# Optimization experiments

Measured on AMD Instinct MI355X. Metric: run time of the kernel, lower is better.

## Reference

```python
import jax, jax.numpy as jnp
import numpy as np

B, L, D, H = 2, 2048, 2048, 16
DH = D // H

def setup_inputs() -> dict:
    key = jax.random.key(0)
    ks = jax.random.split(key, 12)
    def w(k):
        return jax.random.normal(k, (D, D), dtype=jnp.float32) * 0.02
    def b(k):
        return jax.random.normal(k, (D,), dtype=jnp.float32) * 0.02
    return {
        'q': jax.random.normal(ks[0], (B, L, D), dtype=jnp.float32),
        'k': jax.random.normal(ks[1], (B, L, D), dtype=jnp.float32),
        'v': jax.random.normal(ks[2], (B, L, D), dtype=jnp.float32),
        'Wq': w(ks[3]), 'bq': b(ks[4]),
        'Wk': w(ks[5]), 'bk': b(ks[6]),
        'Wv': w(ks[7]), 'bv': b(ks[8]),
        'Wo': w(ks[9]), 'bo': b(ks[10]),
    }

def reference(q, k, v, Wq, bq, Wk, bk, Wv, bv, Wo, bo):
    # Linear projections (torch Linear: x @ W.T + b)
    qh = q @ Wq.T + bq
    kh = k @ Wk.T + bk
    vh = v @ Wv.T + bv
    # b l (h d) -> b h l d
    def split(x):
        b_, l_, _ = x.shape
        return x.reshape(b_, l_, H, DH).transpose(0, 2, 1, 3)
    qh, kh, vh = split(qh), split(kh), split(vh)
    # Faithful to source: scores = q @ k^T / d_head**(-0.5) == q @ k^T * sqrt(d_head)
    scale = jnp.float32(DH) ** 0.5
    scores = jnp.einsum('bhid,bhjd->bhij', qh, kh) * scale
    causal = jnp.triu(jnp.ones((L, L), dtype=jnp.float32), 1)  # triu(1) mask
    scores = scores - causal * 1e7
    attn = jax.nn.softmax(scores, axis=-1)
    out = jnp.einsum('bhij,bhjd->bhid', attn, vh)
    out = out.transpose(0, 2, 1, 3).reshape(B, L, D)  # b h l d -> b l (h d)
    return out @ Wo.T + bo
```

## Files before the change

### kernel.cpp

```cpp
#include <hip/hip_runtime.h>

typedef unsigned short u16;
typedef _Float16 hfrag __attribute__((ext_vector_type(8)));
typedef float f32x4 __attribute__((ext_vector_type(4)));

#define MFMA16F __builtin_amdgcn_mfma_f32_16x16x32_f16

__device__ __forceinline__ u16 f2h(float f) {
  return __builtin_bit_cast(u16, (_Float16)f);
}
__device__ __forceinline__ void splith(float x, u16 &h, u16 &l) {
  _Float16 hh = (_Float16)x;
  _Float16 ll = (_Float16)(x - (float)hh);
  h = __builtin_bit_cast(u16, hh);
  l = __builtin_bit_cast(u16, ll);
}

__device__ __forceinline__ void gl2lds16(const void* g, void* l) {
  __builtin_amdgcn_global_load_lds(
      (const __attribute__((address_space(1))) unsigned int*)g,
      (__attribute__((address_space(3))) unsigned int*)l, 16, 0, 0);
}

__global__ void precvt_h(const float* __restrict__ W, u16* __restrict__ hi)
{
  size_t i = ((size_t)blockIdx.x * 256 + threadIdx.x) * 4;
  float4 x = *(const float4*)(W + i);
  ushort4 h;
  h.x = f2h(x.x); h.y = f2h(x.y); h.z = f2h(x.z); h.w = f2h(x.w);
  *(ushort4*)(hi + i) = h;
}

template<int EMIT>
__global__ __launch_bounds__(256, 2)
void gemm_qk(const float* __restrict__ A, const u16* __restrict__ Wh_g,
             const float* __restrict__ bias,
             u16* __restrict__ ohi, u16* __restrict__ olo)
{
  __shared__ u16 Ahi[128][40];
  __shared__ u16 Alo[128][40];
  __shared__ u16 Whs[128 * 32];

  const int tid = threadIdx.x, wave = tid >> 6, lane = tid & 63;
  const int quad = lane >> 4, l16 = lane & 15;
  const int bm = blockIdx.y * 128, bn = blockIdx.x * 128;
  const int wm = (wave >> 1) * 64, wn = (wave & 1) * 64;
  const int rl = lane >> 2, cb = lane & 3;

  f32x4 acc[4][4] = {};

  for (int k0 = 0; k0 < 2048; k0 += 32) {
    __syncthreads();
#pragma unroll
    for (int i = 0; i < 2; ++i) {
      int r0 = wave * 32 + i * 16;
      gl2lds16(Wh_g + (size_t)(bn + r0 + rl) * 2048 + k0 + cb * 8,
               &Whs[r0 * 32]);
    }
#pragma unroll
    for (int it = 0; it < 4; ++it) {
      int idx = tid + it * 256;
      int row = idx >> 3, c4 = (idx & 7) << 2;
      float4 av = *(const float4*)(A + (size_t)(bm + row) * 2048 + k0 + c4);
      ushort4 h, l;
      splith(av.x, h.x, l.x); splith(av.y, h.y, l.y);
      splith(av.z, h.z, l.z); splith(av.w, h.w, l.w);
      *(ushort4*)&Ahi[row][c4] = h;
      *(ushort4*)&Alo[row][c4] = l;
    }
    __syncthreads();

    hfrag ah[4], al_[4], wh[4];
#pragma unroll
    for (int i = 0; i < 4; ++i) {
      ah[i]  = *(const hfrag*)&Ahi[wm + i * 16 + l16][quad * 8];
      al_[i] = *(const hfrag*)&Alo[wm + i * 16 + l16][quad * 8];
      wh[i]  = *(const hfrag*)&Whs[(wn + i * 16 + l16) * 32 + quad * 8];
    }
#pragma unroll
    for (int mi = 0; mi < 4; ++mi)
#pragma unroll
      for (int ni = 0; ni < 4; ++ni) {
        acc[mi][ni] = MFMA16F(ah[mi],  wh[ni], acc[mi][ni], 0, 0, 0);
        acc[mi][ni] = MFMA16F(al_[mi], wh[ni], acc[mi][ni], 0, 0, 0);
      }
  }

  const float SCALE = 11.31370849898476f;
#pragma unroll
  for (int ni = 0; ni < 4; ++ni) {
    int n_g = bn + wn + ni * 16 + l16;
    float bv = bias[n_g];
#pragma unroll
    for (int mi = 0; mi < 4; ++mi)
#pragma unroll
      for (int r = 0; r < 4; ++r) {
        int m_g = bm + wm + mi * 16 + quad * 4 + r;
        float v = acc[mi][ni][r] + bv;
        int b = m_g >> 11, ll = m_g & 2047, hh = n_g >> 7, dh = n_g & 127;
        size_t off = (((size_t)(b * 16 + hh)) * 2048 + ll) * 128 + dh;
        if constexpr (EMIT == 0) {
          v *= SCALE;
          u16 h, l; splith(v, h, l);
          ohi[off] = h; olo[off] = l;
        } else {
          ohi[off] = f2h(v);
        }
      }
  }
}

template<int AMODE, int OUTM>
__global__ __launch_bounds__(256, 2)
void gemm_pl(const void* __restrict__ Ap, const float* __restrict__ W,
             const float* __restrict__ bias, void* __restrict__ outp)
{
  __shared__ u16 As[128 * 40];
  __shared__ u16 Ws[128][40];

  const int tid = threadIdx.x, wave = tid >> 6, lane = tid & 63;
  const int quad = lane >> 4, l16 = lane & 15;
  const int bm = blockIdx.y * 128, bn = blockIdx.x * 128;
  const int wm = (wave >> 1) * 64, wn = (wave & 1) * 64;
  const int rl = lane >> 2, cb = lane & 3;
  constexpr int ASTRIDE = (AMODE == 1) ? 32 : 40;

  f32x4 acc[4][4] = {};

  for (int k0 = 0; k0 < 2048; k0 += 32) {
    __syncthreads();
    if constexpr (AMODE == 1) {
      const u16* Ah = (const u16*)Ap;
#pragma unroll
      for (int i = 0; i < 2; ++i) {
        int r0 = wave * 32 + i * 16;
        gl2lds16(Ah + (size_t)(bm + r0 + rl) * 2048 + k0 + cb * 8,
                 &As[r0 * 32]);
      }
    }
#pragma unroll
    for (int it = 0; it < 4; ++it) {
      int idx = tid + it * 256;
      int row = idx >> 3, c4 = (idx & 7) << 2;
      float4 wv = *(const float4*)(W + (size_t)(bn + row) * 2048 + k0 + c4);
      ushort4 h;
      h.x = f2h(wv.x); h.y = f2h(wv.y); h.z = f2h(wv.z); h.w = f2h(wv.w);
      *(ushort4*)&Ws[row][c4] = h;
      if constexpr (AMODE == 0) {
        const float* A = (const float*)Ap;
        float4 av = *(const float4*)(A + (size_t)(bm + row) * 2048 + k0 + c4);
        ushort4 ha;
        ha.x = f2h(av.x); ha.y = f2h(av.y); ha.z = f2h(av.z); ha.w = f2h(av.w);
        *(ushort4*)&As[row * 40 + c4] = ha;
      }
    }
    __syncthreads();

    hfrag af[4], wf[4];
#pragma unroll
    for (int i = 0; i < 4; ++i) {
      af[i] = *(const hfrag*)&As[(wm + i * 16 + l16) * ASTRIDE + quad * 8];
      wf[i] = *(const hfrag*)&Ws[wn + i * 16 + l16][quad * 8];
    }
    if constexpr (OUTM == 1) {
#pragma unroll
      for (int mi = 0; mi < 4; ++mi)
#pragma unroll
        for (int ni = 0; ni < 4; ++ni)
          acc[mi][ni] = MFMA16F(wf[mi], af[ni], acc[mi][ni], 0, 0, 0);
    } else {
#pragma unroll
      for (int mi = 0; mi < 4; ++mi)
#pragma unroll
        for (int ni = 0; ni < 4; ++ni)
          acc[mi][ni] = MFMA16F(af[mi], wf[ni], acc[mi][ni], 0, 0, 0);
    }
  }

  if constexpr (OUTM == 1) {
#pragma unroll
    for (int mi = 0; mi < 4; ++mi)
#pragma unroll
      for (int r = 0; r < 4; ++r) {
        int dim = bn + wn + mi * 16 + quad * 4 + r;
        float bv = bias[dim];
        int hh = dim >> 7, dh = dim & 127;
#pragma unroll
        for (int ni = 0; ni < 4; ++ni) {
          int tok = bm + wm + ni * 16 + l16;
          int b = tok >> 11, l = tok & 2047;
          ((u16*)outp)[(((size_t)(b * 16 + hh)) * 128 + dh) * 2048 + l] =
              f2h(acc[mi][ni][r] + bv);
        }
      }
  } else {
#pragma unroll
    for (int ni = 0; ni < 4; ++ni) {
      int n_g = bn + wn + ni * 16 + l16;
      float bv = bias[n_g];
#pragma unroll
      for (int mi = 0; mi < 4; ++mi)
#pragma unroll
        for (int r = 0; r < 4; ++r) {
          int m_g = bm + wm + mi * 16 + quad * 4 + r;
          ((float*)outp)[(size_t)m_g * 2048 + n_g] = acc[mi][ni][r] + bv;
        }
    }
  }
}

__global__ __launch_bounds__(256, 1)
void attn_k(const u16* __restrict__ qhi_g, const u16* __restrict__ qlo_g,
            const u16* __restrict__ khi_g, const u16* __restrict__ vT,
            u16* __restrict__ Ow)
{
  __shared__ u16 KhiB[2][64 * 128];
  __shared__ u16 VTB[2][128 * 64];
  __shared__ u16 PmA[4][32][72];

  const int tid = threadIdx.x, wave = tid >> 6, lane = tid & 63;
  const int quad = lane >> 4, l16 = lane & 15;
  const int bh = blockIdx.x & 31, qx = blockIdx.x >> 5;
  const u16* Qhb = qhi_g + (size_t)bh * 2048 * 128;
  const u16* Qlb = qlo_g + (size_t)bh * 2048 * 128;
  const u16* Khb = khi_g + (size_t)bh * 2048 * 128;
  const u16* Vb  = vT    + (size_t)bh * 128 * 2048;

  const int krl = lane >> 4, kpb = lane & 15;
  const int vrl = lane >> 3, vpb = lane & 7;

  hfrag ones;
#pragma unroll
  for (int j = 0; j < 8; ++j) ones[j] = (_Float16)1.0f;

  auto stage = [&](int kv0, int bsel) {
#pragma unroll
    for (int i = 0; i < 4; ++i) {
      int r = wave * 16 + i * 4 + krl;
      int j = kpb ^ (r & 15);
      gl2lds16(Khb + (size_t)(kv0 + r) * 128 + j * 8,
               &KhiB[bsel][(wave * 16 + i * 4) * 128]);
      int rv = wave * 32 + i * 8 + vrl;
      int jv = vpb ^ (rv & 7);
      gl2lds16(Vb + (size_t)rv * 2048 + kv0 + jv * 8,
               &VTB[bsel][(wave * 32 + i * 8) * 64]);
    }
  };

  const int b = bh >> 4, h = bh & 15;

#pragma unroll 1
  for (int ph = 0; ph < 2; ++ph) {
    const int qt = (ph == 0) ? qx : 15 - qx;
    const int qrow0 = qt * 128 + wave * 32;
    const int nkv = 2 * (qt + 1);

    stage(0, 0);

    hfrag qhf[2][4], qlf[2][4];
#pragma unroll
    for (int t = 0; t < 2; ++t)
#pragma unroll
      for (int f = 0; f < 4; ++f) {
        size_t off = (size_t)(qrow0 + t * 16 + l16) * 128 + f * 32 + quad * 8;
        qhf[t][f] = *(const hfrag*)(Qhb + off);
        qlf[t][f] = *(const hfrag*)(Qlb + off);
      }

    float mprev[2] = {-3e38f, -3e38f};
    f32x4 o[2][9] = {};

#pragma unroll 1
    for (int kt = 0; kt < nkv; ++kt) {
      const int kv0 = kt * 64, bsel = kt & 1;
      __syncthreads();
      if (kt + 1 < nkv) stage((kt + 1) * 64, 1 - bsel);

      if (kv0 <= qrow0 + 31) {
        f32x4 st[4][2] = {};
#pragma unroll
        for (int f = 0; f < 4; ++f)
#pragma unroll
          for (int c = 0; c < 4; ++c) {
            int poff = (c * 16 + l16) * 128 + (((f * 4 + quad) ^ l16) << 3);
            hfrag kf = *(const hfrag*)&KhiB[bsel][poff];
#pragma unroll
            for (int t = 0; t < 2; ++t) {
              st[c][t] = MFMA16F(kf, qhf[t][f], st[c][t], 0, 0, 0);
              st[c][t] = MFMA16F(kf, qlf[t][f], st[c][t], 0, 0, 0);
            }
          }

        const bool needmask = (kv0 + 64 > qrow0);
        float al2[2];
#pragma unroll
        for (int t = 0; t < 2; ++t) {
          const int rg = qrow0 + t * 16 + l16;
          if (needmask) {
#pragma unroll
            for (int c = 0; c < 4; ++c)
#pragma unroll
              for (int r = 0; r < 4; ++r)
                if (kv0 + c * 16 + quad * 4 + r > rg) st[c][t][r] = -1e7f;
          }
          float mx = st[0][t][0];
#pragma unroll
          for (int c = 0; c < 4; ++c)
#pragma unroll
            for (int r = 0; r < 4; ++r) mx = fmaxf(mx, st[c][t][r]);
          mx = fmaxf(mx, __shfl_xor(mx, 16));
          mx = fmaxf(mx, __shfl_xor(mx, 32));
          float mnew = fmaxf(mprev[t], mx);
          al2[t] = __expf(mprev[t] - mnew);
          mprev[t] = mnew;
#pragma unroll
          for (int c = 0; c < 4; ++c) {
            ushort4 pk;
            pk.x = f2h(__expf(st[c][t][0] - mnew));
            pk.y = f2h(__expf(st[c][t][1] - mnew));
            pk.z = f2h(__expf(st[c][t][2] - mnew));
            pk.w = f2h(__expf(st[c][t][3] - mnew));
            *(ushort4*)&PmA[wave][t * 16 + l16][c * 16 + quad * 4] = pk;
          }
        }
        if (__ballot(al2[0] != 1.f || al2[1] != 1.f)) {
#pragma unroll
          for (int t = 0; t < 2; ++t) {
            f32x4 av;
            av[0] = __shfl(al2[t], quad * 4 + 0);
            av[1] = __shfl(al2[t], quad * 4 + 1);
            av[2] = __shfl(al2[t], quad * 4 + 2);
            av[3] = __shfl(al2[t], quad * 4 + 3);
#pragma unroll
            for (int d = 0; d < 9; ++d) o[t][d] *= av;
          }
        }

#pragma unroll
        for (int k2 = 0; k2 < 2; ++k2) {
          hfrag pf0 = *(const hfrag*)&PmA[wave][l16][k2 * 32 + quad * 8];
          hfrag pf1 = *(const hfrag*)&PmA[wave][16 + l16][k2 * 32 + quad * 8];
#pragma unroll
          for (int d = 0; d < 9; ++d) {
            hfrag vf = (d < 8)
                ? *(const hfrag*)&VTB[bsel][(d * 16 + l16) * 64 +
                                            (((k2 * 4 + quad) ^ (l16 & 7)) << 3)]
                : ones;
            o[0][d] = MFMA16F(pf0, vf, o[0][d], 0, 0, 0);
            o[1][d] = MFMA16F(pf1, vf, o[1][d], 0, 0, 0);
          }
        }
      }
    }

#pragma unroll
    for (int t = 0; t < 2; ++t)
#pragma unroll
      for (int r = 0; r < 4; ++r) {
        int rg = qrow0 + t * 16 + quad * 4 + r;
        float inv = 1.f / o[t][8][r];
#pragma unroll
        for (int d = 0; d < 8; ++d)
          Ow[((size_t)(b * 2048 + rg)) * 2048 + h * 128 + d * 16 + l16] =
              f2h(o[t][d][r] * inv);
      }
  }
}

extern "C" void kernel_launch(void* const* d_in, const int* in_sizes, int n_in,
                              void* d_out, int out_size, void* d_ws, size_t ws_size,
                              hipStream_t stream) {
  const float* q  = (const float*)d_in[0];
  const float* k  = (const float*)d_in[1];
  const float* v  = (const float*)d_in[2];
  const float* Wq = (const float*)d_in[3];
  const float* bq = (const float*)d_in[4];
  const float* Wk = (const float*)d_in[5];
  const float* bk = (const float*)d_in[6];
  const float* Wv = (const float*)d_in[7];
  const float* bv = (const float*)d_in[8];
  const float* Wo = (const float*)d_in[9];
  const float* bo = (const float*)d_in[10];

  u16* ws  = (u16*)d_ws;
  u16* qHi = ws;
  u16* qLo = ws + 8388608u;
  u16* kHi = ws + 16777216u;
  u16* WH  = ws + 25165824u;
  u16* vTb = ws + 29360128u;
  u16* Owb = ws + 37748736u;

  dim3 blk(256);
  dim3 gg(16, 32);
  precvt_h<<<4096, blk, 0, stream>>>(Wq, WH);
  gemm_qk<0><<<gg, blk, 0, stream>>>(q, WH, bq, qHi, qLo);
  precvt_h<<<4096, blk, 0, stream>>>(Wk, WH);
  gemm_qk<1><<<gg, blk, 0, stream>>>(k, WH, bk, kHi, nullptr);
  gemm_pl<0, 1><<<gg, blk, 0, stream>>>(v, Wv, bv, vTb);
  attn_k<<<dim3(256), blk, 0, stream>>>(qHi, qLo, kHi, vTb, Owb);
  gemm_pl<1, 2><<<gg, blk, 0, stream>>>(Owb, Wo, bo, d_out);
}
```

Measured before the change: 638.6 us.

## Pre-convert activations to fp16 and stream all GEMM tiles via async LDS loads

Moves the fp32-to-fp16 (hi/lo split) conversion of q, k, v and all weights into separate pre-conversion kernels. Every GEMM then loads both operands with direct global-to-LDS async copies into XOR-swizzled 64-wide K tiles, halving the number of K iterations and barriers. This removes in-loop conversion ALU work and register staging, in exchange for extra full passes over the activations and extra workspace traffic, with buffers reused across stages.

Result: faster. 530.7 us (-16.9%).

```diff
diff --git a/kernel.cpp b/kernel.cpp
--- a/kernel.cpp
+++ b/kernel.cpp
@@ -31,59 +31,68 @@
   *(ushort4*)(hi + i) = h;
 }
 
+__global__ void precvt_split(const float* __restrict__ X,
+                             u16* __restrict__ hi, u16* __restrict__ lo)
+{
+  size_t i = ((size_t)blockIdx.x * 256 + threadIdx.x) * 4;
+  float4 x = *(const float4*)(X + i);
+  ushort4 h, l;
+  splith(x.x, h.x, l.x); splith(x.y, h.y, l.y);
+  splith(x.z, h.z, l.z); splith(x.w, h.w, l.w);
+  *(ushort4*)(hi + i) = h;
+  *(ushort4*)(lo + i) = l;
+}
+
 template<int EMIT>
 __global__ __launch_bounds__(256, 2)
-void gemm_qk(const float* __restrict__ A, const u16* __restrict__ Wh_g,
-             const float* __restrict__ bias,
+void gemm_qk(const u16* __restrict__ Ahi_g, const u16* __restrict__ Alo_g,
+             const u16* __restrict__ Wh_g, const float* __restrict__ bias,
              u16* __restrict__ ohi, u16* __restrict__ olo)
 {
-  __shared__ u16 Ahi[128][40];
-  __shared__ u16 Alo[128][40];
-  __shared__ u16 Whs[128 * 32];
+  __shared__ u16 AhS[128 * 64];
+  __shared__ u16 AlS[128 * 64];
+  __shared__ u16 WS[128 * 64];
 
   const int tid = threadIdx.x, wave = tid >> 6, lane = tid & 63;
   const int quad = lane >> 4, l16 = lane & 15;
   const int bm = blockIdx.y * 128, bn = blockIdx.x * 128;
   const int wm = (wave >> 1) * 64, wn = (wave & 1) * 64;
-  const int rl = lane >> 2, cb = lane & 3;
+  const int srow = lane >> 3;
+  const int jcol = ((lane & 7) ^ srow) << 3;
 
   f32x4 acc[4][4] = {};
 
-  for (int k0 = 0; k0 < 2048; k0 += 32) {
+  for (int k0 = 0; k0 < 2048; k0 += 64) {
     __syncthreads();
 #pragma unroll
-    for (int i = 0; i < 2; ++i) {
-      int r0 = wave * 32 + i * 16;
-      gl2lds16(Wh_g + (size_t)(bn + r0 + rl) * 2048 + k0 + cb * 8,
-               &Whs[r0 * 32]);
-    }
-#pragma unroll
-    for (int it = 0; it < 4; ++it) {
-      int idx = tid + it * 256;
-      int row = idx >> 3, c4 = (idx & 7) << 2;
-      float4 av = *(const float4*)(A + (size_t)(bm + row) * 2048 + k0 + c4);
-      ushort4 h, l;
-      splith(av.x, h.x, l.x); splith(av.y, h.y, l.y);
-      splith(av.z, h.z, l.z); splith(av.w, h.w, l.w);
-      *(ushort4*)&Ahi[row][c4] = h;
-      *(ushort4*)&Alo[row][c4] = l;
+    for (int i = 0; i < 4; ++i) {
+      int r0 = wave * 32 + i * 8;
+      size_t ga = (size_t)(bm + r0 + srow) * 2048 + k0 + jcol;
+      size_t gw = (size_t)(bn + r0 + srow) * 2048 + k0 + jcol;
+      gl2lds16(Ahi_g + ga, &AhS[r0 * 64]);
+      gl2lds16(Alo_g + ga, &AlS[r0 * 64]);
+      gl2lds16(Wh_g + gw, &WS[r0 * 64]);
     }
     __syncthreads();
 
-    hfrag ah[4], al_[4], wh[4];
-#pragma unroll
-    for (int i = 0; i < 4; ++i) {
-      ah[i]  = *(const hfrag*)&Ahi[wm + i * 16 + l16][quad * 8];
-      al_[i] = *(const hfrag*)&Alo[wm + i * 16 + l16][quad * 8];
-      wh[i]  = *(const hfrag*)&Whs[(wn + i * 16 + l16) * 32 + quad * 8];
-    }
-#pragma unroll
-    for (int mi = 0; mi < 4; ++mi)
-#pragma unroll
-      for (int ni = 0; ni < 4; ++ni) {
-        acc[mi][ni] = MFMA16F(ah[mi],  wh[ni], acc[mi][ni], 0, 0, 0);
-        acc[mi][ni] = MFMA16F(al_[mi], wh[ni], acc[mi][ni], 0, 0, 0);
-      }
+#pragma unroll
+    for (int kk = 0; kk < 2; ++kk) {
+      const int jr = (((kk * 4 + quad) ^ (l16 & 7)) << 3);
+      hfrag ah[4], al_[4], wh[4];
+#pragma unroll
+      for (int i = 0; i < 4; ++i) {
+        ah[i]  = *(const hfrag*)&AhS[(wm + i * 16 + l16) * 64 + jr];
+        al_[i] = *(const hfrag*)&AlS[(wm + i * 16 + l16) * 64 + jr];
+        wh[i]  = *(const hfrag*)&WS[(wn + i * 16 + l16) * 64 + jr];
+      }
+#pragma unroll
+      for (int mi = 0; mi < 4; ++mi)
+#pragma unroll
+        for (int ni = 0; ni < 4; ++ni) {
+          acc[mi][ni] = MFMA16F(ah[mi],  wh[ni], acc[mi][ni], 0, 0, 0);
+          acc[mi][ni] = MFMA16F(al_[mi], wh[ni], acc[mi][ni], 0, 0, 0);
+        }
+    }
   }
 
   const float SCALE = 11.31370849898476f;
@@ -110,70 +119,55 @@
   }
 }
 
-template<int AMODE, int OUTM>
+template<int OUTM>
 __global__ __launch_bounds__(256, 2)
-void gemm_pl(const void* __restrict__ Ap, const float* __restrict__ W,
+void gemm_pl(const u16* __restrict__ A_g, const u16* __restrict__ Wh_g,
              const float* __restrict__ bias, void* __restrict__ outp)
 {
-  __shared__ u16 As[128 * 40];
-  __shared__ u16 Ws[128][40];
+  __shared__ u16 AS[128 * 64];
+  __shared__ u16 WS[128 * 64];
 
   const int tid = threadIdx.x, wave = tid >> 6, lane = tid & 63;
   const int quad = lane >> 4, l16 = lane & 15;
   const int bm = blockIdx.y * 128, bn = blockIdx.x * 128;
   const int wm = (wave >> 1) * 64, wn = (wave & 1) * 64;
-  const int rl = lane >> 2, cb = lane & 3;
-  constexpr int ASTRIDE = (AMODE == 1) ? 32 : 40;
+  const int srow = lane >> 3;
+  const int jcol = ((lane & 7) ^ srow) << 3;
 
   f32x4 acc[4][4] = {};
 
-  for (int k0 = 0; k0 < 2048; k0 += 32) {
+  for (int k0 = 0; k0 < 2048; k0 += 64) {
     __syncthreads();
-    if constexpr (AMODE == 1) {
-      const u16* Ah = (const u16*)Ap;
-#pragma unroll
-      for (int i = 0; i < 2; ++i) {
-        int r0 = wave * 32 + i * 16;
-        gl2lds16(Ah + (size_t)(bm + r0 + rl) * 2048 + k0 + cb * 8,
-                 &As[r0 * 32]);
-      }
-    }
-#pragma unroll
-    for (int it = 0; it < 4; ++it) {
-      int idx = tid + it * 256;
-      int row = idx >> 3, c4 = (idx & 7) << 2;
-      float4 wv = *(const float4*)(W + (size_t)(bn + row) * 2048 + k0 + c4);
-      ushort4 h;
-      h.x = f2h(wv.x); h.y = f2h(wv.y); h.z = f2h(wv.z); h.w = f2h(wv.w);
-      *(ushort4*)&Ws[row][c4] = h;
-      if constexpr (AMODE == 0) {
-        const float* A = (const float*)Ap;
-        float4 av = *(const float4*)(A + (size_t)(bm + row) * 2048 + k0 + c4);
-        ushort4 ha;
-        ha.x = f2h(av.x); ha.y = f2h(av.y); ha.z = f2h(av.z); ha.w = f2h(av.w);
-        *(ushort4*)&As[row * 40 + c4] = ha;
-      }
+#pragma unroll
+    for (int i = 0; i < 4; ++i) {
+      int r0 = wave * 32 + i * 8;
+      gl2lds16(A_g  + (size_t)(bm + r0 + srow) * 2048 + k0 + jcol, &AS[r0 * 64]);
+      gl2lds16(Wh_g + (size_t)(bn + r0 + srow) * 2048 + k0 + jcol, &WS[r0 * 64]);
     }
     __syncthreads();
 
-    hfrag af[4], wf[4];
-#pragma unroll
-    for (int i = 0; i < 4; ++i) {
-      af[i] = *(const hfrag*)&As[(wm + i * 16 + l16) * ASTRIDE + quad * 8];
-      wf[i] = *(const hfrag*)&Ws[wn + i * 16 + l16][quad * 8];
-    }
-    if constexpr (OUTM == 1) {
-#pragma unroll
-      for (int mi = 0; mi < 4; ++mi)
-#pragma unroll
-        for (int ni = 0; ni < 4; ++ni)
-          acc[mi][ni] = MFMA16F(wf[mi], af[ni], acc[mi][ni], 0, 0, 0);
-    } else {
-#pragma unroll
-      for (int mi = 0; mi < 4; ++mi)
-#pragma unroll
-        for (int ni = 0; ni < 4; ++ni)
-          acc[mi][ni] = MFMA16F(af[mi], wf[ni], acc[mi][ni], 0, 0, 0);
+#pragma unroll
+    for (int kk = 0; kk < 2; ++kk) {
+      const int jr = (((kk * 4 + quad) ^ (l16 & 7)) << 3);
+      hfrag af[4], wf[4];
+#pragma unroll
+      for (int i = 0; i < 4; ++i) {
+        af[i] = *(const hfrag*)&AS[(wm + i * 16 + l16) * 64 + jr];
+        wf[i] = *(const hfrag*)&WS[(wn + i * 16 + l16) * 64 + jr];
+      }
+      if constexpr (OUTM == 1) {
+#pragma unroll
+        for (int mi = 0; mi < 4; ++mi)
+#pragma unroll
+          for (int ni = 0; ni < 4; ++ni)
+            acc[mi][ni] = MFMA16F(wf[mi], af[ni], acc[mi][ni], 0, 0, 0);
+      } else {
+#pragma unroll
+        for (int mi = 0; mi < 4; ++mi)
+#pragma unroll
+          for (int ni = 0; ni < 4; ++ni)
+            acc[mi][ni] = MFMA16F(af[mi], wf[ni], acc[mi][ni], 0, 0, 0);
+      }
     }
   }
 
@@ -382,21 +376,27 @@
   const float* Wo = (const float*)d_in[9];
   const float* bo = (const float*)d_in[10];
 
-  u16* ws  = (u16*)d_ws;
-  u16* qHi = ws;
-  u16* qLo = ws + 8388608u;
-  u16* kHi = ws + 16777216u;
-  u16* WH  = ws + 25165824u;
-  u16* vTb = ws + 29360128u;
-  u16* Owb = ws + 37748736u;
+  u16* ws   = (u16*)d_ws;
+  u16* qHi  = ws;
+  u16* qLo  = ws + 8388608u;
+  u16* kHi  = ws + 16777216u;
+  u16* WH   = ws + 25165824u;
+  u16* bufA = ws + 29360128u;
+  u16* bufB = ws + 37748736u;
 
   dim3 blk(256);
   dim3 gg(16, 32);
+
+  precvt_split<<<8192, blk, 0, stream>>>(q, bufA, bufB);
   precvt_h<<<4096, blk, 0, stream>>>(Wq, WH);
-  gemm_qk<0><<<gg, blk, 0, stream>>>(q, WH, bq, qHi, qLo);
+  gemm_qk<0><<<gg, blk, 0, stream>>>(bufA, bufB, WH, bq, qHi, qLo);
+  precvt_split<<<8192, blk, 0, stream>>>(k, bufA, bufB);
   precvt_h<<<4096, blk, 0, stream>>>(Wk, WH);
-  gemm_qk<1><<<gg, blk, 0, stream>>>(k, WH, bk, kHi, nullptr);
-  gemm_pl<0, 1><<<gg, blk, 0, stream>>>(v, Wv, bv, vTb);
-  attn_k<<<dim3(256), blk, 0, stream>>>(qHi, qLo, kHi, vTb, Owb);
-  gemm_pl<1, 2><<<gg, blk, 0, stream>>>(Owb, Wo, bo, d_out);
-}
+  gemm_qk<1><<<gg, blk, 0, stream>>>(bufA, bufB, WH, bk, kHi, nullptr);
+  precvt_h<<<8192, blk, 0, stream>>>(v, bufA);
+  precvt_h<<<4096, blk, 0, stream>>>(Wv, WH);
+  gemm_pl<1><<<gg, blk, 0, stream>>>(bufA, WH, bv, bufB);
+  attn_k<<<dim3(256), blk, 0, stream>>>(qHi, qLo, kHi, bufB, bufA);
+  precvt_h<<<4096, blk, 0, stream>>>(Wo, WH);
+  gemm_pl<2><<<gg, blk, 0, stream>>>(bufA, WH, bo, d_out);
+}
```
